# Kernel optimization log

Measured on AMD Instinct MI355X. Metric: run time of the kernel, lower is better.

## Reference

```python
import jax, jax.numpy as jnp
import numpy as np

TAU = 1.0
EPS = 1e-8  # torch cosine_similarity norm clamp


def setup_inputs() -> dict:
    key = jax.random.key(0)
    k1, k2, k3 = jax.random.split(key, 3)
    B, d, M, C = 4096, 128, 8192, 16
    f = jax.random.normal(k1, (B, d), dtype=jnp.float32)
    f_neg = jax.random.normal(k2, (M, d), dtype=jnp.float32)
    labels = jax.random.randint(k3, (B,), 0, C, dtype=jnp.int64)
    return {"f": f, "f_neg": f_neg, "labels": labels, "batch_size": B}


def _normalize(x):
    n = jnp.linalg.norm(x, axis=-1, keepdims=True)
    return x / jnp.maximum(n, EPS)


def reference(f, f_neg, labels, batch_size):
    B = batch_size
    fn = _normalize(f)            # [B, d]
    gn = _normalize(f_neg)        # [M, d]

    sim_bb = jnp.einsum('id,jd->ij', fn, fn)   # [B, B] cosine sims in-batch
    sim_bn = jnp.einsum('id,md->im', fn, gn)   # [B, M] sims with neg bank

    offdiag = ~jnp.eye(B, dtype=bool)                       # exclude self
    pos_mask = (labels[:, None] == labels[None, :]) & offdiag  # [B, B]

    exp_bb = jnp.exp(sim_bb / TAU) * offdiag                # self row removed
    exp_bn = jnp.exp(sim_bn / TAU)
    # denominator_i = sum over all non-self in-batch + all bank negatives
    denom = exp_bb.sum(axis=1) + exp_bn.sum(axis=1)         # [B]

    # -log(exp(s_p/tau)/denom) = log(denom) - s_p/tau, averaged over positives
    neg_log = jnp.log(denom)[:, None] - sim_bb / TAU        # [B, B]
    n_pos = pos_mask.sum(axis=1)                            # [B]
    loss_i = jnp.sum(jnp.where(pos_mask, neg_log, 0.0), axis=1) / n_pos

    return jnp.sum(loss_i) / B  # reduction='mean'
```

## Files before the change

### kernel.cpp

```cpp
#include <hip/hip_runtime.h>
#include <hip/hip_bf16.h>
#include <hip/hip_fp8.h>

#define B_ROWS 4096
#define D_K    128
#define M_ROWS 8192
#define N_TOT  12288
#define NCHUNK 32
#define JT_PER_CHUNK 6
#define JCOLS  64
#define NCLS   16

typedef __attribute__((ext_vector_type(4))) int   intx4;
typedef __attribute__((ext_vector_type(8))) int   intx8;
typedef __attribute__((ext_vector_type(4))) float floatx4;

__global__ __launch_bounds__(256) void nrm_kernel(
    const float* __restrict__ f, const float* __restrict__ fneg,
    unsigned char* __restrict__ G8, float* __restrict__ S,
    int* __restrict__ hist, float* __restrict__ out)
{
    const int tid  = threadIdx.x;
    const int wave = tid >> 6;
    const int lane = tid & 63;
    const int row  = blockIdx.x * 4 + wave;
    if (blockIdx.x == 0) {
        #pragma unroll
        for (int k = 0; k < 8; ++k) S[tid + k * 256] = 0.f;
        if (tid < NCLS) hist[tid] = 0;
        if (tid == 0) out[0] = 0.f;
    }
    const float* src = (row < B_ROWS) ? (f + (size_t)row * D_K)
                                      : (fneg + (size_t)(row - B_ROWS) * D_K);
    float2 v = *reinterpret_cast<const float2*>(src + lane * 2);
    float ss = v.x * v.x + v.y * v.y;
    #pragma unroll
    for (int m = 1; m < 64; m <<= 1) ss += __shfl_xor(ss, m, 64);
    const float scale = 1.0f / fmaxf(sqrtf(ss), 1e-8f);
    __hip_fp8_e4m3 q0(v.x * scale);
    __hip_fp8_e4m3 q1(v.y * scale);
    const unsigned short pk =
        (unsigned short)q0.__x | ((unsigned short)q1.__x << 8);
    *reinterpret_cast<unsigned short*>(G8 + (size_t)row * D_K + lane * 2) = pk;
}

__global__ __launch_bounds__(256) void csum_kernel(
    const unsigned char* __restrict__ G8, const int* __restrict__ labels,
    float* __restrict__ S, int* __restrict__ hist)
{
    __shared__ float Sp[NCLS * 32];
    __shared__ int   lh[NCLS];
    const int tid    = threadIdx.x;
    const int stripe = blockIdx.x & 31;
    const int dc     = blockIdx.x >> 5;
    #pragma unroll
    for (int k = tid; k < NCLS * 32; k += 256) Sp[k] = 0.f;
    if (tid < NCLS) lh[tid] = 0;
    __syncthreads();

    const int j0 = stripe * 128;
    if (dc == 0 && tid < 128) atomicAdd(&lh[labels[j0 + tid]], 1);

    const int d = tid & 31;
    const int w = tid >> 5;
    for (int jj = w; jj < 128; jj += 8) {
        const int j = j0 + jj;
        const int c = labels[j];
        const float v = float(reinterpret_cast<const __hip_fp8_e4m3&>(
            G8[(size_t)j * D_K + dc * 32 + d]));
        atomicAdd(&Sp[c * 32 + d], v);
    }
    __syncthreads();
    for (int k = tid; k < NCLS * 32; k += 256) {
        const int c  = k >> 5;
        const int dd = k & 31;
        atomicAdd(&S[c * D_K + dc * 32 + dd], Sp[k]);
    }
    if (dc == 0 && tid < NCLS) atomicAdd(&hist[tid], lh[tid]);
}

__global__ __launch_bounds__(256, 4) void sim_kernel(
    const unsigned char* __restrict__ G8, float* __restrict__ part_d)
{
    __shared__ unsigned char Bs[2][JCOLS * D_K];

    const int jc   = blockIdx.x;
    const int it   = blockIdx.y;
    const int tid  = threadIdx.x;
    const int wave = tid >> 6;
    const int lane = tid & 63;
    const int i0   = it * 128 + wave * 32;

    const int r16 = lane & 15;
    const int grp = lane >> 4;

    const unsigned char* Abase = G8 + (size_t)(i0 + r16) * D_K + grp * 32;
    intx8 afr[2];
    #pragma unroll
    for (int a = 0; a < 2; ++a)
        afr[a] = *reinterpret_cast<const intx8*>(Abase + (size_t)a * 16 * D_K);

    float dsum[2][4];
    #pragma unroll
    for (int a = 0; a < 2; ++a)
        #pragma unroll
        for (int r = 0; r < 4; ++r) dsum[a][r] = 0.f;

    int srcoff[2];
    #pragma unroll
    for (int s = 0; s < 2; ++s) {
        const int row  = s * 32 + (tid >> 3);
        const int gran = (tid & 7) ^ (row & 7);
        srcoff[s] = row * D_K + gran * 16;
    }

    intx4 streg[2];
    {
        const unsigned char* src =
            G8 + (size_t)(jc * JT_PER_CHUNK) * JCOLS * D_K;
        #pragma unroll
        for (int s = 0; s < 2; ++s)
            streg[s] = *reinterpret_cast<const intx4*>(src + srcoff[s]);
        #pragma unroll
        for (int s = 0; s < 2; ++s)
            *reinterpret_cast<intx4*>(&Bs[0][0] + s * 4096 + tid * 16) =
                streg[s];
    }

    for (int t = 0; t < JT_PER_CHUNK; ++t) {
        const int cur = t & 1;
        __syncthreads();

        if (t + 1 < JT_PER_CHUNK) {
            const unsigned char* src =
                G8 + (size_t)(jc * JT_PER_CHUNK + t + 1) * JCOLS * D_K;
            #pragma unroll
            for (int s = 0; s < 2; ++s)
                streg[s] = *reinterpret_cast<const intx4*>(src + srcoff[s]);
        }

        floatx4 acc[2][4];
        #pragma unroll
        for (int a = 0; a < 2; ++a)
            #pragma unroll
            for (int b = 0; b < 4; ++b)
                acc[a][b] = (floatx4){0.f, 0.f, 0.f, 0.f};

        const unsigned char* base = &Bs[cur][0];
        #pragma unroll
        for (int b = 0; b < 4; ++b) {
            const int jloc = b * 16 + r16;
            const int sw   = jloc & 7;
            intx4 lo = *reinterpret_cast<const intx4*>(
                base + jloc * D_K + ((2 * grp)     ^ sw) * 16);
            intx4 hi = *reinterpret_cast<const intx4*>(
                base + jloc * D_K + ((2 * grp + 1) ^ sw) * 16);
            intx8 bfr;
            #pragma unroll
            for (int e = 0; e < 4; ++e) { bfr[e] = lo[e]; bfr[e + 4] = hi[e]; }
            #pragma unroll
            for (int a = 0; a < 2; ++a)
                acc[a][b] = __builtin_amdgcn_mfma_scale_f32_16x16x128_f8f6f4(
                    afr[a], bfr, acc[a][b], 0, 0,
                    0, 0x7F7F7F7F, 0, 0x7F7F7F7F);
        }

        #pragma unroll
        for (int a = 0; a < 2; ++a)
            #pragma unroll
            for (int r = 0; r < 4; ++r) {
                float s0 = __expf(acc[a][0][r]) + __expf(acc[a][1][r]);
                float s1 = __expf(acc[a][2][r]) + __expf(acc[a][3][r]);
                dsum[a][r] += s0 + s1;
            }

        if (t + 1 < JT_PER_CHUNK) {
            #pragma unroll
            for (int s = 0; s < 2; ++s)
                *reinterpret_cast<intx4*>(
                    &Bs[cur ^ 1][0] + s * 4096 + tid * 16) = streg[s];
        }
    }

    #pragma unroll
    for (int a = 0; a < 2; ++a)
        #pragma unroll
        for (int r = 0; r < 4; ++r) {
            #pragma unroll
            for (int m = 1; m < 16; m <<= 1)
                dsum[a][r] += __shfl_xor(dsum[a][r], m, 64);
        }
    if (r16 == 0) {
        #pragma unroll
        for (int a = 0; a < 2; ++a)
            #pragma unroll
            for (int r = 0; r < 4; ++r)
                part_d[(size_t)(i0 + a * 16 + grp * 4 + r) * NCHUNK + jc] =
                    dsum[a][r];
    }
}

__global__ __launch_bounds__(256) void fin_kernel(
    const unsigned char* __restrict__ G8, const float* __restrict__ part_d,
    const float* __restrict__ S, const int* __restrict__ labels,
    const int* __restrict__ hist, float* __restrict__ out)
{
    const int tid  = threadIdx.x;
    const int wave = tid >> 6;
    const int lane = tid & 63;

    float lsum = 0.f;
    #pragma unroll 2
    for (int rr = 0; rr < 8; ++rr) {
        const int i   = (blockIdx.x * 4 + wave) * 8 + rr;
        const int lab = labels[i];
        float pd = (lane < NCHUNK) ? part_d[(size_t)i * NCHUNK + lane] : 0.f;
        const unsigned char* gr = G8 + (size_t)i * D_K + lane * 2;
        const float f0 = float(reinterpret_cast<const __hip_fp8_e4m3&>(gr[0]));
        const float f1 = float(reinterpret_cast<const __hip_fp8_e4m3&>(gr[1]));
        float2 sv = *reinterpret_cast<const float2*>(S + lab * D_K + lane * 2);
        float self = f0 * f0 + f1 * f1;
        float sp   = f0 * sv.x + f1 * sv.y;
        #pragma unroll
        for (int m = 1; m < 64; m <<= 1) {
            pd   += __shfl_xor(pd, m, 64);
            self += __shfl_xor(self, m, 64);
            sp   += __shfl_xor(sp, m, 64);
        }
        if (lane == 0) {
            const float npos  = (float)(hist[lab] - 1);
            const float denom = pd - __expf(self);
            lsum += __logf(denom) - (sp - self) / npos;
        }
    }
    __shared__ float w4[4];
    if (lane == 0) w4[wave] = lsum;
    __syncthreads();
    if (tid == 0)
        atomicAdd(out, (w4[0] + w4[1] + w4[2] + w4[3]) * (1.0f / (float)B_ROWS));
}

extern "C" void kernel_launch(void* const* d_in, const int* in_sizes, int n_in,
                              void* d_out, int out_size, void* d_ws, size_t ws_size,
                              hipStream_t stream) {
    const float* f      = (const float*)d_in[0];
    const float* fneg   = (const float*)d_in[1];
    const int*   labels = (const int*)d_in[2];
    float*       out    = (float*)d_out;

    char* ws = (char*)d_ws;
    unsigned char* G8     = (unsigned char*)(ws);
    float*         part_d = (float*)(ws + 1572864);
    float*         S      = (float*)(ws + 1572864 + 524288);
    int*           hist   = (int*)(ws + 1572864 + 524288 + 8192);

    nrm_kernel<<<N_TOT / 4, 256, 0, stream>>>(f, fneg, G8, S, hist, out);
    csum_kernel<<<128, 256, 0, stream>>>(G8, labels, S, hist);

    dim3 gridS(NCHUNK, 32);
    sim_kernel<<<gridS, 256, 0, stream>>>(G8, part_d);

    fin_kernel<<<128, 256, 0, stream>>>(G8, part_d, S, labels, hist, out);
}
```

Before: 37.13 us.

## Load B fragments directly from global memory instead of staging through LDS

Removes the double-buffered shared-memory staging of the negative/batch feature tiles in the similarity kernel. Each wave now reads its MFMA B fragments straight from global memory (relying on L2/L1 caching), which drops the __syncthreads barriers and LDS traffic. The trade-off is that the four waves in a block redundantly fetch the same B data from cache, and load latency is less hidden (only unroll 2).

```diff
diff --git a/kernel.cpp b/kernel.cpp
--- a/kernel.cpp
+++ b/kernel.cpp
@@ -7,11 +7,9 @@
 #define M_ROWS 8192
 #define N_TOT  12288
 #define NCHUNK 32
-#define JT_PER_CHUNK 6
-#define JCOLS  64
+#define JFRAG  24
 #define NCLS   16
 
-typedef __attribute__((ext_vector_type(4))) int   intx4;
 typedef __attribute__((ext_vector_type(8))) int   intx8;
 typedef __attribute__((ext_vector_type(4))) float floatx4;
 
@@ -82,8 +80,6 @@
 __global__ __launch_bounds__(256, 4) void sim_kernel(
     const unsigned char* __restrict__ G8, float* __restrict__ part_d)
 {
-    __shared__ unsigned char Bs[2][JCOLS * D_K];
-
     const int jc   = blockIdx.x;
     const int it   = blockIdx.y;
     const int tid  = threadIdx.x;
@@ -106,80 +102,24 @@
         #pragma unroll
         for (int r = 0; r < 4; ++r) dsum[a][r] = 0.f;
 
-    int srcoff[2];
-    #pragma unroll
-    for (int s = 0; s < 2; ++s) {
-        const int row  = s * 32 + (tid >> 3);
-        const int gran = (tid & 7) ^ (row & 7);
-        srcoff[s] = row * D_K + gran * 16;
-    }
-
-    intx4 streg[2];
-    {
-        const unsigned char* src =
-            G8 + (size_t)(jc * JT_PER_CHUNK) * JCOLS * D_K;
-        #pragma unroll
-        for (int s = 0; s < 2; ++s)
-            streg[s] = *reinterpret_cast<const intx4*>(src + srcoff[s]);
-        #pragma unroll
-        for (int s = 0; s < 2; ++s)
-            *reinterpret_cast<intx4*>(&Bs[0][0] + s * 4096 + tid * 16) =
-                streg[s];
-    }
-
-    for (int t = 0; t < JT_PER_CHUNK; ++t) {
-        const int cur = t & 1;
-        __syncthreads();
-
-        if (t + 1 < JT_PER_CHUNK) {
-            const unsigned char* src =
-                G8 + (size_t)(jc * JT_PER_CHUNK + t + 1) * JCOLS * D_K;
-            #pragma unroll
-            for (int s = 0; s < 2; ++s)
-                streg[s] = *reinterpret_cast<const intx4*>(src + srcoff[s]);
-        }
-
-        floatx4 acc[2][4];
+    const unsigned char* Bbase =
+        G8 + (size_t)(jc * (JFRAG * 16) + r16) * D_K + grp * 32;
+
+    #pragma unroll 2
+    for (int t = 0; t < JFRAG; ++t) {
+        const intx8 bfr = *reinterpret_cast<const intx8*>(
+            Bbase + (size_t)t * 16 * D_K);
+        floatx4 acc[2];
+        #pragma unroll
+        for (int a = 0; a < 2; ++a)
+            acc[a] = __builtin_amdgcn_mfma_scale_f32_16x16x128_f8f6f4(
+                afr[a], bfr, (floatx4){0.f, 0.f, 0.f, 0.f}, 0, 0,
+                0, 0x7F7F7F7F, 0, 0x7F7F7F7F);
         #pragma unroll
         for (int a = 0; a < 2; ++a)
             #pragma unroll
-            for (int b = 0; b < 4; ++b)
-                acc[a][b] = (floatx4){0.f, 0.f, 0.f, 0.f};
-
-        const unsigned char* base = &Bs[cur][0];
-        #pragma unroll
-        for (int b = 0; b < 4; ++b) {
-            const int jloc = b * 16 + r16;
-            const int sw   = jloc & 7;
-            intx4 lo = *reinterpret_cast<const intx4*>(
-                base + jloc * D_K + ((2 * grp)     ^ sw) * 16);
-            intx4 hi = *reinterpret_cast<const intx4*>(
-                base + jloc * D_K + ((2 * grp + 1) ^ sw) * 16);
-            intx8 bfr;
-            #pragma unroll
-            for (int e = 0; e < 4; ++e) { bfr[e] = lo[e]; bfr[e + 4] = hi[e]; }
-            #pragma unroll
-            for (int a = 0; a < 2; ++a)
-                acc[a][b] = __builtin_amdgcn_mfma_scale_f32_16x16x128_f8f6f4(
-                    afr[a], bfr, acc[a][b], 0, 0,
-                    0, 0x7F7F7F7F, 0, 0x7F7F7F7F);
-        }
-
-        #pragma unroll
-        for (int a = 0; a < 2; ++a)
-            #pragma unroll
-            for (int r = 0; r < 4; ++r) {
-                float s0 = __expf(acc[a][0][r]) + __expf(acc[a][1][r]);
-                float s1 = __expf(acc[a][2][r]) + __expf(acc[a][3][r]);
-                dsum[a][r] += s0 + s1;
-            }
-
-        if (t + 1 < JT_PER_CHUNK) {
-            #pragma unroll
-            for (int s = 0; s < 2; ++s)
-                *reinterpret_cast<intx4*>(
-                    &Bs[cur ^ 1][0] + s * 4096 + tid * 16) = streg[s];
-        }
+            for (int r = 0; r < 4; ++r)
+                dsum[a][r] += __expf(acc[a][r]);
     }
 
     #pragma unroll
```

Result: slower. 50.73 us (+36.6%).

## Fuse class-sum into normalize kernel and fold reductions into sim launch

Applied to the files above, without the earlier changes.

Merges the normalization and per-class column-sum kernels: each normalize block handles 32 rows, and the first 128 blocks write per-block class partial sums from the quantized values they already hold. The final reduction of those partials, the label histogram and the zeroing of the output are moved into an extra row of blocks in the sim kernel grid. The fin kernel now processes 16 rows per wave with half as many blocks. This removes one kernel launch and the global atomics. In exchange it adds a serial 128-step reduction in a few blocks and an extra 1 MB partial buffer.

```diff
diff --git a/kernel.cpp b/kernel.cpp
--- a/kernel.cpp
+++ b/kernel.cpp
@@ -10,83 +10,104 @@
 #define JT_PER_CHUNK 6
 #define JCOLS  64
 #define NCLS   16
+#define NRMB   384
+#define NBIB   128
 
 typedef __attribute__((ext_vector_type(4))) int   intx4;
 typedef __attribute__((ext_vector_type(8))) int   intx8;
 typedef __attribute__((ext_vector_type(4))) float floatx4;
 
-__global__ __launch_bounds__(256) void nrm_kernel(
+__device__ __forceinline__ float fp8_to_f32(unsigned char b) {
+    __hip_fp8_e4m3 h; h.__x = b; return float(h);
+}
+
+__global__ __launch_bounds__(256) void nrmS_kernel(
     const float* __restrict__ f, const float* __restrict__ fneg,
-    unsigned char* __restrict__ G8, float* __restrict__ S,
-    int* __restrict__ hist, float* __restrict__ out)
+    const int* __restrict__ labels, unsigned char* __restrict__ G8,
+    float* __restrict__ partS)
 {
     const int tid  = threadIdx.x;
     const int wave = tid >> 6;
     const int lane = tid & 63;
-    const int row  = blockIdx.x * 4 + wave;
-    if (blockIdx.x == 0) {
-        #pragma unroll
-        for (int k = 0; k < 8; ++k) S[tid + k * 256] = 0.f;
-        if (tid < NCLS) hist[tid] = 0;
-        if (tid == 0) out[0] = 0.f;
-    }
-    const float* src = (row < B_ROWS) ? (f + (size_t)row * D_K)
-                                      : (fneg + (size_t)(row - B_ROWS) * D_K);
-    float2 v = *reinterpret_cast<const float2*>(src + lane * 2);
-    float ss = v.x * v.x + v.y * v.y;
-    #pragma unroll
-    for (int m = 1; m < 64; m <<= 1) ss += __shfl_xor(ss, m, 64);
-    const float scale = 1.0f / fmaxf(sqrtf(ss), 1e-8f);
-    __hip_fp8_e4m3 q0(v.x * scale);
-    __hip_fp8_e4m3 q1(v.y * scale);
-    const unsigned short pk =
-        (unsigned short)q0.__x | ((unsigned short)q1.__x << 8);
-    *reinterpret_cast<unsigned short*>(G8 + (size_t)row * D_K + lane * 2) = pk;
-}
-
-__global__ __launch_bounds__(256) void csum_kernel(
+    const int blk  = blockIdx.x;
+    const int rbase = blk * 32 + wave * 8;
+
+    float2 v[8];
+    #pragma unroll
+    for (int r = 0; r < 8; ++r) {
+        const int row = rbase + r;
+        const float* src = (row < B_ROWS)
+            ? (f + (size_t)row * D_K) : (fneg + (size_t)(row - B_ROWS) * D_K);
+        v[r] = *reinterpret_cast<const float2*>(src + lane * 2);
+    }
+
+    unsigned short q[8];
+    int cls[8];
+    #pragma unroll
+    for (int r = 0; r < 8; ++r) {
+        const int row = rbase + r;
+        float ss = v[r].x * v[r].x + v[r].y * v[r].y;
+        #pragma unroll
+        for (int m = 1; m < 64; m <<= 1) ss += __shfl_xor(ss, m, 64);
+        const float scale = 1.0f / fmaxf(sqrtf(ss), 1e-8f);
+        __hip_fp8_e4m3 q0(v[r].x * scale);
+        __hip_fp8_e4m3 q1(v[r].y * scale);
+        const unsigned short pk =
+            (unsigned short)q0.__x | ((unsigned short)q1.__x << 8);
+        *reinterpret_cast<unsigned short*>(G8 + (size_t)row * D_K + lane * 2) = pk;
+        q[r]   = pk;
+        cls[r] = (row < B_ROWS) ? labels[row] : 0;
+    }
+
+    if (blk < NBIB) {
+        __shared__ float Sp[NCLS * D_K];
+        for (int k = tid; k < NCLS * D_K; k += 256) Sp[k] = 0.f;
+        __syncthreads();
+        #pragma unroll
+        for (int r = 0; r < 8; ++r) {
+            atomicAdd(&Sp[cls[r] * D_K + 2 * lane],     fp8_to_f32(q[r] & 0xff));
+            atomicAdd(&Sp[cls[r] * D_K + 2 * lane + 1], fp8_to_f32(q[r] >> 8));
+        }
+        __syncthreads();
+        #pragma unroll
+        for (int k = 0; k < 8; ++k)
+            partS[(size_t)blk * (NCLS * D_K) + tid * 8 + k] = Sp[tid * 8 + k];
+    }
+}
+
+__global__ __launch_bounds__(256, 4) void sim_kernel(
     const unsigned char* __restrict__ G8, const int* __restrict__ labels,
-    float* __restrict__ S, int* __restrict__ hist)
-{
-    __shared__ float Sp[NCLS * 32];
-    __shared__ int   lh[NCLS];
-    const int tid    = threadIdx.x;
-    const int stripe = blockIdx.x & 31;
-    const int dc     = blockIdx.x >> 5;
-    #pragma unroll
-    for (int k = tid; k < NCLS * 32; k += 256) Sp[k] = 0.f;
-    if (tid < NCLS) lh[tid] = 0;
-    __syncthreads();
-
-    const int j0 = stripe * 128;
-    if (dc == 0 && tid < 128) atomicAdd(&lh[labels[j0 + tid]], 1);
-
-    const int d = tid & 31;
-    const int w = tid >> 5;
-    for (int jj = w; jj < 128; jj += 8) {
-        const int j = j0 + jj;
-        const int c = labels[j];
-        const float v = float(reinterpret_cast<const __hip_fp8_e4m3&>(
-            G8[(size_t)j * D_K + dc * 32 + d]));
-        atomicAdd(&Sp[c * 32 + d], v);
-    }
-    __syncthreads();
-    for (int k = tid; k < NCLS * 32; k += 256) {
-        const int c  = k >> 5;
-        const int dd = k & 31;
-        atomicAdd(&S[c * D_K + dc * 32 + dd], Sp[k]);
-    }
-    if (dc == 0 && tid < NCLS) atomicAdd(&hist[tid], lh[tid]);
-}
-
-__global__ __launch_bounds__(256, 4) void sim_kernel(
-    const unsigned char* __restrict__ G8, float* __restrict__ part_d)
+    const float* __restrict__ partS, float* __restrict__ part_d,
+    float* __restrict__ S, int* __restrict__ hist, float* __restrict__ out)
 {
     __shared__ unsigned char Bs[2][JCOLS * D_K];
 
+    const int tid = threadIdx.x;
+
+    if (blockIdx.y == 32) {
+        const int role = blockIdx.x;
+        if (role < 16) {
+            if (tid < 128) {
+                const int e = role * 128 + tid;
+                float s = 0.f;
+                for (int b = 0; b < NBIB; ++b)
+                    s += partS[(size_t)b * (NCLS * D_K) + e];
+                S[e] = s;
+            }
+        } else if (role == 16) {
+            __shared__ int lh[NCLS];
+            if (tid < NCLS) lh[tid] = 0;
+            __syncthreads();
+            for (int j = tid; j < B_ROWS; j += 256) atomicAdd(&lh[labels[j]], 1);
+            __syncthreads();
+            if (tid < NCLS) hist[tid] = lh[tid];
+            if (tid == 0) out[0] = 0.f;
+        }
+        return;
+    }
+
     const int jc   = blockIdx.x;
     const int it   = blockIdx.y;
-    const int tid  = threadIdx.x;
     const int wave = tid >> 6;
     const int lane = tid & 63;
     const int i0   = it * 128 + wave * 32;
@@ -211,13 +232,13 @@
 
     float lsum = 0.f;
     #pragma unroll 2
-    for (int rr = 0; rr < 8; ++rr) {
-        const int i   = (blockIdx.x * 4 + wave) * 8 + rr;
+    for (int rr = 0; rr < 16; ++rr) {
+        const int i   = (blockIdx.x * 4 + wave) * 16 + rr;
         const int lab = labels[i];
         float pd = (lane < NCHUNK) ? part_d[(size_t)i * NCHUNK + lane] : 0.f;
         const unsigned char* gr = G8 + (size_t)i * D_K + lane * 2;
-        const float f0 = float(reinterpret_cast<const __hip_fp8_e4m3&>(gr[0]));
-        const float f1 = float(reinterpret_cast<const __hip_fp8_e4m3&>(gr[1]));
+        const float f0 = fp8_to_f32(gr[0]);
+        const float f1 = fp8_to_f32(gr[1]);
         float2 sv = *reinterpret_cast<const float2*>(S + lab * D_K + lane * 2);
         float self = f0 * f0 + f1 * f1;
         float sp   = f0 * sv.x + f1 * sv.y;
@@ -251,14 +272,14 @@
     char* ws = (char*)d_ws;
     unsigned char* G8     = (unsigned char*)(ws);
     float*         part_d = (float*)(ws + 1572864);
-    float*         S      = (float*)(ws + 1572864 + 524288);
-    int*           hist   = (int*)(ws + 1572864 + 524288 + 8192);
-
-    nrm_kernel<<<N_TOT / 4, 256, 0, stream>>>(f, fneg, G8, S, hist, out);
-    csum_kernel<<<128, 256, 0, stream>>>(G8, labels, S, hist);
-
-    dim3 gridS(NCHUNK, 32);
-    sim_kernel<<<gridS, 256, 0, stream>>>(G8, part_d);
-
-    fin_kernel<<<128, 256, 0, stream>>>(G8, part_d, S, labels, hist, out);
-}
+    float*         partS  = (float*)(ws + 1572864 + 524288);
+    float*         S      = (float*)(ws + 1572864 + 524288 + 1048576);
+    int*           hist   = (int*)(ws + 1572864 + 524288 + 1048576 + 8192);
+
+    nrmS_kernel<<<NRMB, 256, 0, stream>>>(f, fneg, labels, G8, partS);
+
+    dim3 gridS(NCHUNK, 33);
+    sim_kernel<<<gridS, 256, 0, stream>>>(G8, labels, partS, part_d, S, hist, out);
+
+    fin_kernel<<<64, 256, 0, stream>>>(G8, part_d, S, labels, hist, out);
+}
```

After: 43.36 us. 16.8% more time.

## Fold class-sum kernel into sim grid and prescale A by log2e for exp2

Applied to the files above, without the earlier changes.

Removes the separate csum kernel launch by adding extra blocks (blockIdx.y >= 32) to the similarity grid that compute per-class feature sums and label histogram, reusing the shared buffer. Also writes a second fp8 copy of the batch rows prescaled by log2(e) so the sim kernel can use exp2f instead of __expf, removing a multiply per element. The extra quantized copy introduces slightly different rounding in the exponent argument, and costs an extra workspace write and buffer.

```diff
diff --git a/kernel.cpp b/kernel.cpp
--- a/kernel.cpp
+++ b/kernel.cpp
@@ -15,10 +15,14 @@
 typedef __attribute__((ext_vector_type(8))) int   intx8;
 typedef __attribute__((ext_vector_type(4))) float floatx4;
 
+__device__ __forceinline__ float fp8_to_f32(unsigned char b) {
+    __hip_fp8_e4m3 h; h.__x = b; return float(h);
+}
+
 __global__ __launch_bounds__(256) void nrm_kernel(
     const float* __restrict__ f, const float* __restrict__ fneg,
-    unsigned char* __restrict__ G8, float* __restrict__ S,
-    int* __restrict__ hist, float* __restrict__ out)
+    unsigned char* __restrict__ G8, unsigned char* __restrict__ A8,
+    float* __restrict__ S, int* __restrict__ hist, float* __restrict__ out)
 {
     const int tid  = threadIdx.x;
     const int wave = tid >> 6;
@@ -42,51 +46,55 @@
     const unsigned short pk =
         (unsigned short)q0.__x | ((unsigned short)q1.__x << 8);
     *reinterpret_cast<unsigned short*>(G8 + (size_t)row * D_K + lane * 2) = pk;
-}
-
-__global__ __launch_bounds__(256) void csum_kernel(
-    const unsigned char* __restrict__ G8, const int* __restrict__ labels,
+    if (row < B_ROWS) {
+        const float s2 = scale * 1.44269504f;
+        __hip_fp8_e4m3 a0(v.x * s2);
+        __hip_fp8_e4m3 a1(v.y * s2);
+        const unsigned short pa =
+            (unsigned short)a0.__x | ((unsigned short)a1.__x << 8);
+        *reinterpret_cast<unsigned short*>(A8 + (size_t)row * D_K + lane * 2) = pa;
+    }
+}
+
+__global__ __launch_bounds__(256, 4) void sim_kernel(
+    const unsigned char* __restrict__ G8, const unsigned char* __restrict__ A8,
+    const int* __restrict__ labels, float* __restrict__ part_d,
     float* __restrict__ S, int* __restrict__ hist)
 {
-    __shared__ float Sp[NCLS * 32];
-    __shared__ int   lh[NCLS];
-    const int tid    = threadIdx.x;
-    const int stripe = blockIdx.x & 31;
-    const int dc     = blockIdx.x >> 5;
-    #pragma unroll
-    for (int k = tid; k < NCLS * 32; k += 256) Sp[k] = 0.f;
-    if (tid < NCLS) lh[tid] = 0;
-    __syncthreads();
-
-    const int j0 = stripe * 128;
-    if (dc == 0 && tid < 128) atomicAdd(&lh[labels[j0 + tid]], 1);
-
-    const int d = tid & 31;
-    const int w = tid >> 5;
-    for (int jj = w; jj < 128; jj += 8) {
-        const int j = j0 + jj;
-        const int c = labels[j];
-        const float v = float(reinterpret_cast<const __hip_fp8_e4m3&>(
-            G8[(size_t)j * D_K + dc * 32 + d]));
-        atomicAdd(&Sp[c * 32 + d], v);
-    }
-    __syncthreads();
-    for (int k = tid; k < NCLS * 32; k += 256) {
-        const int c  = k >> 5;
-        const int dd = k & 31;
-        atomicAdd(&S[c * D_K + dc * 32 + dd], Sp[k]);
-    }
-    if (dc == 0 && tid < NCLS) atomicAdd(&hist[tid], lh[tid]);
-}
-
-__global__ __launch_bounds__(256, 4) void sim_kernel(
-    const unsigned char* __restrict__ G8, float* __restrict__ part_d)
-{
     __shared__ unsigned char Bs[2][JCOLS * D_K];
+
+    const int tid = threadIdx.x;
+
+    if (blockIdx.y >= 32) {
+        const int svc    = (blockIdx.y - 32) * NCHUNK + blockIdx.x;
+        const int stripe = svc & 31;
+        const int dc     = svc >> 5;
+        float* Sp = (float*)&Bs[0][0];
+        int*   lh = (int*)(Sp + NCLS * 32);
+        for (int k = tid; k < NCLS * 32; k += 256) Sp[k] = 0.f;
+        if (tid < NCLS) lh[tid] = 0;
+        __syncthreads();
+
+        const int j0 = stripe * 128;
+        if (dc == 0 && tid < 128) atomicAdd(&lh[labels[j0 + tid]], 1);
+
+        const int d = tid & 31;
+        const int w = tid >> 5;
+        for (int jj = w; jj < 128; jj += 8) {
+            const int j = j0 + jj;
+            const int c = labels[j];
+            atomicAdd(&Sp[c * 32 + d],
+                      fp8_to_f32(G8[(size_t)j * D_K + dc * 32 + d]));
+        }
+        __syncthreads();
+        for (int k = tid; k < NCLS * 32; k += 256)
+            atomicAdd(&S[(k >> 5) * D_K + dc * 32 + (k & 31)], Sp[k]);
+        if (dc == 0 && tid < NCLS) atomicAdd(&hist[tid], lh[tid]);
+        return;
+    }
 
     const int jc   = blockIdx.x;
     const int it   = blockIdx.y;
-    const int tid  = threadIdx.x;
     const int wave = tid >> 6;
     const int lane = tid & 63;
     const int i0   = it * 128 + wave * 32;
@@ -94,7 +102,7 @@
     const int r16 = lane & 15;
     const int grp = lane >> 4;
 
-    const unsigned char* Abase = G8 + (size_t)(i0 + r16) * D_K + grp * 32;
+    const unsigned char* Abase = A8 + (size_t)(i0 + r16) * D_K + grp * 32;
     intx8 afr[2];
     #pragma unroll
     for (int a = 0; a < 2; ++a)
@@ -169,8 +177,8 @@
         for (int a = 0; a < 2; ++a)
             #pragma unroll
             for (int r = 0; r < 4; ++r) {
-                float s0 = __expf(acc[a][0][r]) + __expf(acc[a][1][r]);
-                float s1 = __expf(acc[a][2][r]) + __expf(acc[a][3][r]);
+                float s0 = exp2f(acc[a][0][r]) + exp2f(acc[a][1][r]);
+                float s1 = exp2f(acc[a][2][r]) + exp2f(acc[a][3][r]);
                 dsum[a][r] += s0 + s1;
             }
 
@@ -216,8 +224,8 @@
         const int lab = labels[i];
         float pd = (lane < NCHUNK) ? part_d[(size_t)i * NCHUNK + lane] : 0.f;
         const unsigned char* gr = G8 + (size_t)i * D_K + lane * 2;
-        const float f0 = float(reinterpret_cast<const __hip_fp8_e4m3&>(gr[0]));
-        const float f1 = float(reinterpret_cast<const __hip_fp8_e4m3&>(gr[1]));
+        const float f0 = fp8_to_f32(gr[0]);
+        const float f1 = fp8_to_f32(gr[1]);
         float2 sv = *reinterpret_cast<const float2*>(S + lab * D_K + lane * 2);
         float self = f0 * f0 + f1 * f1;
         float sp   = f0 * sv.x + f1 * sv.y;
@@ -250,15 +258,15 @@
 
     char* ws = (char*)d_ws;
     unsigned char* G8     = (unsigned char*)(ws);
-    float*         part_d = (float*)(ws + 1572864);
-    float*         S      = (float*)(ws + 1572864 + 524288);
-    int*           hist   = (int*)(ws + 1572864 + 524288 + 8192);
-
-    nrm_kernel<<<N_TOT / 4, 256, 0, stream>>>(f, fneg, G8, S, hist, out);
-    csum_kernel<<<128, 256, 0, stream>>>(G8, labels, S, hist);
-
-    dim3 gridS(NCHUNK, 32);
-    sim_kernel<<<gridS, 256, 0, stream>>>(G8, part_d);
+    unsigned char* A8     = (unsigned char*)(ws + 1572864);
+    float*         part_d = (float*)(ws + 1572864 + 524288);
+    float*         S      = (float*)(ws + 1572864 + 524288 + 524288);
+    int*           hist   = (int*)(ws + 1572864 + 524288 + 524288 + 8192);
+
+    nrm_kernel<<<N_TOT / 4, 256, 0, stream>>>(f, fneg, G8, A8, S, hist, out);
+
+    dim3 gridS(NCHUNK, 36);
+    sim_kernel<<<gridS, 256, 0, stream>>>(G8, A8, labels, part_d, S, hist);
 
     fin_kernel<<<128, 256, 0, stream>>>(G8, part_d, S, labels, hist, out);
 }
```

After: 36.17 us. 1.03x faster.
